# Optimization experiments

Measured on AMD Instinct MI355X. Metric: run time of the kernel, lower is better.

Reference implementation:

```python
import jax, jax.numpy as jnp
import numpy as np

B, S, D, H, L, TPB = 4, 1020, 1024, 16, 4, 17
VOBS, VACT = 4096, 16
DH = D // H
EPS = 1e-3  # keras LayerNormalization default epsilon


def _ln(x, g, b):
    m = jnp.mean(x, axis=-1, keepdims=True)
    v = jnp.mean((x - m) ** 2, axis=-1, keepdims=True)
    return (x - m) * jax.lax.rsqrt(v + EPS) * g + b


def setup_inputs() -> dict:
    key = jax.random.key(0)
    ks = iter(jax.random.split(key, 64))
    def p(shape, s=0.02):
        return jax.random.normal(next(ks), shape, jnp.float32) * s
    pos = np.arange(S)
    is_obs = jnp.asarray((pos % TPB) < (TPB - 1))
    tok = jax.random.randint(next(ks), (B, S), 0, VOBS)
    tok = jnp.where(is_obs[None, :], tok, tok % VACT).astype(jnp.int32)
    d = dict(
        tokens=tok,
        pos_emb=p((S, D)), emb_obs=p((VOBS, D)), emb_act=p((VACT, D)),
        ln1_g=jnp.ones((L, D)), ln1_b=jnp.zeros((L, D)),
        wq=p((L, D, D)), bq=jnp.zeros((L, D)),
        wk=p((L, D, D)), bk=jnp.zeros((L, D)),
        wv=p((L, D, D)), bv=jnp.zeros((L, D)),
        wo=p((L, D, D)), bo=jnp.zeros((L, D)),
        ln2_g=jnp.ones((L, D)), ln2_b=jnp.zeros((L, D)),
        w1=p((L, D, 4 * D)), b1=jnp.zeros((L, 4 * D)),
        w2=p((L, 4 * D, D)), b2=jnp.zeros((L, D)),
        lnf_g=jnp.ones((D,)), lnf_b=jnp.zeros((D,)),
        ho1=p((D, D)), bo1=jnp.zeros((D,)),
        ho2=p((D, VOBS)), bo2=jnp.zeros((VOBS,)),
        he1=p((D, D)), be1=jnp.zeros((D,)),
        he2=p((D, 2)), be2=jnp.zeros((2,)),
    )
    return d


def reference(tokens, pos_emb, emb_obs, emb_act, ln1_g, ln1_b, wq, bq, wk, bk,
              wv, bv, wo, bo, ln2_g, ln2_b, w1, b1, w2, b2, lnf_g, lnf_b,
              ho1, bo1, ho2, bo2, he1, be1, he2, be2):
    pos = jnp.arange(S)
    is_obs = (pos % TPB) < (TPB - 1)  # obs positions within each block
    # token embedding: obs table on obs positions, act table on act positions
    x = jnp.where(is_obs[None, :, None],
                  emb_obs[jnp.minimum(tokens, VOBS - 1)],
                  emb_act[jnp.minimum(tokens, VACT - 1)])
    x = x + pos_emb[None]
    neg_mask = (1.0 - jnp.tril(jnp.ones((S, S), jnp.float32))) * -1e9
    inv_sqrt_dk = 1.0 / np.sqrt(DH).astype(np.float32)
    for i in range(L):
        h = _ln(x, ln1_g[i], ln1_b[i])
        q = (h @ wq[i] + bq[i]).reshape(B, S, H, DH).transpose(0, 2, 1, 3)
        k = (h @ wk[i] + bk[i]).reshape(B, S, H, DH).transpose(0, 2, 1, 3)
        v = (h @ wv[i] + bv[i]).reshape(B, S, H, DH).transpose(0, 2, 1, 3)
        scores = jnp.einsum('bhqd,bhkd->bhqk', q, k) * inv_sqrt_dk + neg_mask
        w = jax.nn.softmax(scores, axis=-1)
        o = jnp.einsum('bhqk,bhkd->bhqd', w, v).transpose(0, 2, 1, 3).reshape(B, S, D)
        x = x + (o @ wo[i] + bo[i])
        h = _ln(x, ln2_g[i], ln2_b[i])
        h = jax.nn.gelu(h @ w1[i] + b1[i], approximate=False) @ w2[i] + b2[i]
        x = x + h
    x = _ln(x, lnf_g, lnf_b)
    # head slices (static)
    p_np = np.arange(S)
    head_obs_idx = jnp.asarray(np.nonzero(((p_np + 1) % TPB) != (TPB - 1))[0])  # 960
    act_idx = jnp.asarray(np.nonzero((p_np % TPB) == (TPB - 1))[0])            # 60
    xo = x[:, head_obs_idx]
    logits_obs = jax.nn.relu(xo @ ho1 + bo1) @ ho2 + bo2   # [B, 960, VOBS]
    xe = x[:, act_idx]
    logits_ends = jax.nn.relu(xe @ he1 + be1) @ he2 + be2  # [B, 60, 2]
    return (logits_obs, logits_ends)
```

## Files before the change

kernel.cpp:

```cpp
#include <hip/hip_runtime.h>
#include <hip/hip_bf16.h>
#include <math.h>

namespace {

constexpr int kS = 1020, kD = 1024, kTPB = 17, kDH = 64;
constexpr int kVOBS = 4096, kVACT = 16;
constexpr int kBS = 4080;
constexpr float kEPS = 1e-3f;

typedef float f32x4 __attribute__((ext_vector_type(4)));
typedef __bf16 bfx8 __attribute__((ext_vector_type(8)));
typedef unsigned short u16;
typedef u16 us8 __attribute__((ext_vector_type(8)));
typedef u16 us4 __attribute__((ext_vector_type(4)));

__device__ __forceinline__ float bf2f(u16 u) {
  union { unsigned int i; float f; } v; v.i = (unsigned int)u << 16; return v.f;
}
__device__ __forceinline__ u16 f2bf(float f) {
  union { float f; unsigned int i; } v; v.f = f;
  unsigned int r = v.i + 0x7FFFu + ((v.i >> 16) & 1u);
  return (u16)(r >> 16);
}

__global__ void k_embed(const int* __restrict__ tokens, const float* __restrict__ pos_emb,
                        const float* __restrict__ emb_obs, const float* __restrict__ emb_act,
                        float* __restrict__ x) {
  int bs = blockIdx.x;
  int s = bs % kS;
  int tk = tokens[bs];
  bool obs = (s % kTPB) < (kTPB - 1);
  const float* e;
  if (obs) { int t2 = tk < kVOBS - 1 ? tk : kVOBS - 1; e = emb_obs + (size_t)t2 * kD; }
  else     { int t2 = tk < kVACT - 1 ? tk : kVACT - 1; e = emb_act + (size_t)t2 * kD; }
  int c = threadIdx.x * 4;
  float4 ev = *(const float4*)(e + c);
  float4 pv = *(const float4*)(pos_emb + (size_t)s * kD + c);
  float4 o; o.x = ev.x + pv.x; o.y = ev.y + pv.y; o.z = ev.z + pv.z; o.w = ev.w + pv.w;
  *(float4*)(x + (size_t)bs * kD + c) = o;
}

__global__ void k_pack_bias(const float* __restrict__ bq, const float* __restrict__ bk,
                            const float* __restrict__ bv, float* __restrict__ bqkv) {
  int idx = blockIdx.x * 256 + threadIdx.x;
  int l = idx / 3072, rem = idx % 3072;
  int sel = rem >> 10, cc = rem & 1023;
  const float* src = sel == 0 ? bq : (sel == 1 ? bk : bv);
  bqkv[idx] = src[l * kD + cc];
}

__global__ void k_ln(const float* __restrict__ x, const float* __restrict__ g,
                     const float* __restrict__ b, u16* __restrict__ out) {
  int row = blockIdx.x;
  int t = threadIdx.x;
  const float* xr = x + (size_t)row * kD;
  float4 v = *(const float4*)(xr + t * 4);
  float s1 = v.x + v.y + v.z + v.w;
  float s2 = v.x * v.x + v.y * v.y + v.z * v.z + v.w * v.w;
  #pragma unroll
  for (int m = 32; m; m >>= 1) { s1 += __shfl_xor(s1, m); s2 += __shfl_xor(s2, m); }
  __shared__ float ls1[4], ls2[4];
  int w = t >> 6;
  if ((t & 63) == 0) { ls1[w] = s1; ls2[w] = s2; }
  __syncthreads();
  float S1 = ls1[0] + ls1[1] + ls1[2] + ls1[3];
  float S2 = ls2[0] + ls2[1] + ls2[2] + ls2[3];
  float mean = S1 * (1.0f / kD);
  float var = S2 * (1.0f / kD) - mean * mean;
  float rs = rsqrtf(var + kEPS);
  int c = t * 4;
  float4 gv = *(const float4*)(g + c);
  float4 bv = *(const float4*)(b + c);
  us4 o;
  o[0] = f2bf((v.x - mean) * rs * gv.x + bv.x);
  o[1] = f2bf((v.y - mean) * rs * gv.y + bv.y);
  o[2] = f2bf((v.z - mean) * rs * gv.z + bv.z);
  o[3] = f2bf((v.w - mean) * rs * gv.w + bv.w);
  *(us4*)(out + (size_t)row * kD + c) = o;
}

__global__ void k_transpose(const float* __restrict__ in, u16* __restrict__ out,
                            int R, int C, int ld) {
  __shared__ float tile[32][33];
  int tx = threadIdx.x, ty = threadIdx.y;
  int c0 = blockIdx.x * 32, r0 = blockIdx.y * 32;
  #pragma unroll
  for (int i = 0; i < 4; ++i)
    tile[ty + i * 8][tx] = in[(size_t)(r0 + ty + i * 8) * ld + c0 + tx];
  __syncthreads();
  #pragma unroll
  for (int i = 0; i < 4; ++i)
    out[(size_t)(c0 + ty + i * 8) * R + r0 + tx] = f2bf(tile[tx][ty + i * 8]);
}

template <int EPI, int BM>
__global__ void __launch_bounds__(256)
k_gemm(const u16* __restrict__ A, const u16* __restrict__ Bt, const float* __restrict__ bias,
       const float* __restrict__ resid, void* __restrict__ out, int M, int N, int K, int ldo) {
  constexpr int MFRAG = BM / 32;
  __shared__ alignas(16) u16 As[BM * 32];
  __shared__ alignas(16) u16 Bs[128 * 32];
  int tid = threadIdx.x;
  int nwg = gridDim.x * gridDim.y;
  int lin = blockIdx.y * gridDim.x + blockIdx.x;
  int swzid = (lin & 7) * (nwg >> 3) + (lin >> 3);
  int m0 = (swzid % gridDim.x) * BM;
  int n0 = (swzid / gridDim.x) * 128;
  int lane = tid & 63, wv = tid >> 6;
  int wm = wv >> 1, wn = wv & 1;
  f32x4 acc[MFRAG][4] = {};

  for (int k0 = 0; k0 < K; k0 += 32) {
    #pragma unroll
    for (int n = 0; n < BM / 64; ++n) {
      int u = n * 256 + wv * 64 + lane;
      int r = u >> 2, ch = u & 3;
      int gr = m0 + r; if (gr >= M) gr = M - 1;
      int cg = ch ^ ((r >> 1) & 3);
      const u16* src = A + (size_t)gr * K + k0 + cg * 8;
      __builtin_amdgcn_global_load_lds(
          (const __attribute__((address_space(1))) unsigned int*)src,
          (__attribute__((address_space(3))) unsigned int*)&As[(size_t)(n * 256 + wv * 64) * 8],
          16, 0, 0);
    }
    #pragma unroll
    for (int n = 0; n < 2; ++n) {
      int u = n * 256 + wv * 64 + lane;
      int r = u >> 2, ch = u & 3;
      int cg = ch ^ ((r >> 1) & 3);
      const u16* src = Bt + (size_t)(n0 + r) * K + k0 + cg * 8;
      __builtin_amdgcn_global_load_lds(
          (const __attribute__((address_space(1))) unsigned int*)src,
          (__attribute__((address_space(3))) unsigned int*)&Bs[(size_t)(n * 256 + wv * 64) * 8],
          16, 0, 0);
    }
    __syncthreads();

    bfx8 af[MFRAG], bfr[4];
    int ch = lane >> 4;
    #pragma unroll
    for (int mf = 0; mf < MFRAG; ++mf) {
      int row = wm * (BM / 2) + mf * 16 + (lane & 15);
      af[mf] = *(const bfx8*)(&As[row * 32 + ((ch ^ ((row >> 1) & 3)) << 3)]);
    }
    #pragma unroll
    for (int nf = 0; nf < 4; ++nf) {
      int row = wn * 64 + nf * 16 + (lane & 15);
      bfr[nf] = *(const bfx8*)(&Bs[row * 32 + ((ch ^ ((row >> 1) & 3)) << 3)]);
    }
    #pragma unroll
    for (int mf = 0; mf < MFRAG; ++mf)
      #pragma unroll
      for (int nf = 0; nf < 4; ++nf)
        acc[mf][nf] = __builtin_amdgcn_mfma_f32_16x16x32_bf16(af[mf], bfr[nf], acc[mf][nf], 0, 0, 0);
    __syncthreads();
  }

  #pragma unroll
  for (int mf = 0; mf < MFRAG; ++mf) {
    #pragma unroll
    for (int nf = 0; nf < 4; ++nf) {
      int gcol = n0 + wn * 64 + nf * 16 + (lane & 15);
      float bv = bias ? bias[gcol] : 0.0f;
      #pragma unroll
      for (int r = 0; r < 4; ++r) {
        int grow = m0 + wm * (BM / 2) + mf * 16 + (lane >> 4) * 4 + r;
        if (grow >= M) continue;
        float val = acc[mf][nf][r] + bv;
        size_t off2 = (size_t)grow * ldo + gcol;
        if (EPI == 0) {
          ((u16*)out)[off2] = f2bf(val);
        } else if (EPI == 1) {
          ((u16*)out)[off2] = f2bf(val > 0.f ? val : 0.f);
        } else if (EPI == 2) {
          ((u16*)out)[off2] = f2bf(0.5f * val * (1.f + erff(val * 0.70710678118654752440f)));
        } else if (EPI == 3) {
          ((float*)out)[off2] = resid[off2] + val;
        } else {
          ((float*)out)[off2] = val;
        }
      }
    }
  }
}

__device__ __forceinline__ int swz(int row, int colu16) {
  return (row * 64 + colu16) ^ ((row & 7) << 3) ^ ((row & 24) << 1);
}

__global__ void __launch_bounds__(256)
k_attn(const u16* __restrict__ q, const u16* __restrict__ k, const u16* __restrict__ v,
       u16* __restrict__ o, int ldin) {
  __shared__ u16 Kl[64 * 64];
  __shared__ u16 Vt[64 * 64];
  const int qb = blockIdx.x * 64;
  const int bh = blockIdx.y;
  const int b = bh >> 4, hh = bh & 15;
  const int tid = threadIdx.x;
  const int lane = tid & 63, w = tid >> 6;
  const int g = lane >> 4, c = lane & 15;
  const int q0 = qb + w * 16;
  const size_t base = (size_t)(b * kS) * ldin + hh * kDH;

  bfx8 qf0, qf1;
  {
    int qr = q0 + c; if (qr >= kS) qr = kS - 1;
    const u16* qp = q + base + (size_t)qr * ldin + g * 8;
    qf0 = *(const bfx8*)(qp);
    qf1 = *(const bfx8*)(qp + 32);
  }

  float mst = -1e30f, lsum = 0.f;
  f32x4 ot[4] = {};

  const int ntiles = blockIdx.x + 1;
  for (int t = 0; t < ntiles; ++t) {
    const int kt = t * 64;
    {
      int kr = tid >> 2, ds2 = (tid & 3) * 16;
      int kg = kt + kr; if (kg >= kS) kg = kS - 1;
      const u16* kp = k + base + (size_t)kg * ldin + ds2;
      us8 a0 = *(const us8*)(kp);
      us8 a1 = *(const us8*)(kp + 8);
      *(us8*)(&Kl[swz(kr, ds2)]) = a0;
      *(us8*)(&Kl[swz(kr, ds2 + 8)]) = a1;
      const u16* vp = v + base + (size_t)kg * ldin + ds2;
      us8 b0 = *(const us8*)(vp);
      us8 b1 = *(const us8*)(vp + 8);
      #pragma unroll
      for (int i2 = 0; i2 < 8; ++i2) Vt[swz(ds2 + i2, kr)] = b0[i2];
      #pragma unroll
      for (int i2 = 0; i2 < 8; ++i2) Vt[swz(ds2 + 8 + i2, kr)] = b1[i2];
    }
    __syncthreads();

    f32x4 s[4];
    #pragma unroll
    for (int kb = 0; kb < 4; ++kb) {
      bfx8 kf0 = *(const bfx8*)(&Kl[swz(kb * 16 + c, g * 8)]);
      bfx8 kf1 = *(const bfx8*)(&Kl[swz(kb * 16 + c, g * 8 + 32)]);
      f32x4 acc = {};
      acc = __builtin_amdgcn_mfma_f32_16x16x32_bf16(kf0, qf0, acc, 0, 0, 0);
      acc = __builtin_amdgcn_mfma_f32_16x16x32_bf16(kf1, qf1, acc, 0, 0, 0);
      s[kb] = acc;
    }

    const int qg = q0 + c;
    const bool diag = (kt + 63 > q0);
    float p[4][4];
    float tmax = -1e30f;
    #pragma unroll
    for (int kb = 0; kb < 4; ++kb)
      #pragma unroll
      for (int r = 0; r < 4; ++r) {
        float val = s[kb][r] * 0.125f;
        if (diag && (kt + kb * 16 + g * 4 + r > qg)) val = -1e30f;
        p[kb][r] = val;
        tmax = fmaxf(tmax, val);
      }
    tmax = fmaxf(tmax, __shfl_xor(tmax, 16));
    tmax = fmaxf(tmax, __shfl_xor(tmax, 32));
    float mnew = fmaxf(mst, tmax);
    float alpha = __expf(mst - mnew);
    float psum = 0.f;
    #pragma unroll
    for (int kb = 0; kb < 4; ++kb)
      #pragma unroll
      for (int r = 0; r < 4; ++r) {
        float e = __expf(p[kb][r] - mnew);
        p[kb][r] = e;
        psum += e;
      }
    psum += __shfl_xor(psum, 16);
    psum += __shfl_xor(psum, 32);
    lsum = lsum * alpha + psum;
    mst = mnew;
    #pragma unroll
    for (int db = 0; db < 4; ++db) {
      ot[db][0] *= alpha; ot[db][1] *= alpha;
      ot[db][2] *= alpha; ot[db][3] *= alpha;
    }

    #pragma unroll
    for (int h = 0; h < 2; ++h) {
      bfx8 pf;
      #pragma unroll
      for (int j = 0; j < 8; ++j)
        pf[j] = (__bf16)p[2 * h + (j >> 2)][j & 3];
      #pragma unroll
      for (int db = 0; db < 4; ++db) {
        us4 lo = *(const us4*)(&Vt[swz(16 * db + c, 32 * h + 4 * g)]);
        us4 hi = *(const us4*)(&Vt[swz(16 * db + c, 32 * h + 16 + 4 * g)]);
        union { us8 u; bfx8 bf; } cv;
        cv.u[0] = lo[0]; cv.u[1] = lo[1]; cv.u[2] = lo[2]; cv.u[3] = lo[3];
        cv.u[4] = hi[0]; cv.u[5] = hi[1]; cv.u[6] = hi[2]; cv.u[7] = hi[3];
        ot[db] = __builtin_amdgcn_mfma_f32_16x16x32_bf16(cv.bf, pf, ot[db], 0, 0, 0);
      }
    }
    __syncthreads();
  }

  if (q0 + c < kS) {
    float inv = 1.0f / lsum;
    u16* op = o + (size_t)(b * kS) * kD + hh * kDH + (size_t)(q0 + c) * kD;
    #pragma unroll
    for (int db = 0; db < 4; ++db)
      #pragma unroll
      for (int r = 0; r < 4; ++r)
        op[16 * db + 4 * g + r] = f2bf(ot[db][r] * inv);
  }
}

__global__ void k_gather_obs(const u16* __restrict__ xf, u16* __restrict__ xo) {
  int r = blockIdx.x;
  int b = r / 960, rr = r % 960;
  int j = rr & 15, blk = rr >> 4;
  int s = blk * kTPB + j + (j == 15 ? 1 : 0);
  const unsigned int* src = (const unsigned int*)(xf + ((size_t)(b * kS + s)) * kD);
  unsigned int* dst = (unsigned int*)(xo + (size_t)r * kD);
  dst[threadIdx.x] = src[threadIdx.x];
  dst[threadIdx.x + 256] = src[threadIdx.x + 256];
}
__global__ void k_gather_act(const u16* __restrict__ xf, u16* __restrict__ xe) {
  int r = blockIdx.x;
  int b = r / 60, rr = r % 60;
  int s = rr * kTPB + (kTPB - 1);
  const unsigned int* src = (const unsigned int*)(xf + ((size_t)(b * kS + s)) * kD);
  unsigned int* dst = (unsigned int*)(xe + (size_t)r * kD);
  dst[threadIdx.x] = src[threadIdx.x];
  dst[threadIdx.x + 256] = src[threadIdx.x + 256];
}

__global__ void k_ends(const u16* __restrict__ t2, const float* __restrict__ he2,
                       const float* __restrict__ be2, float* __restrict__ out) {
  int r = blockIdx.x;
  int t = threadIdx.x;
  float p0 = 0.f, p1 = 0.f;
  for (int j = t; j < kD; j += 256) {
    float xv = bf2f(t2[(size_t)r * kD + j]);
    p0 += xv * he2[j * 2];
    p1 += xv * he2[j * 2 + 1];
  }
  #pragma unroll
  for (int msk = 32; msk; msk >>= 1) { p0 += __shfl_xor(p0, msk); p1 += __shfl_xor(p1, msk); }
  __shared__ float l0[4], l1[4];
  int w = t >> 6;
  if ((t & 63) == 0) { l0[w] = p0; l1[w] = p1; }
  __syncthreads();
  if (t == 0) {
    out[r * 2 + 0] = l0[0] + l0[1] + l0[2] + l0[3] + be2[0];
    out[r * 2 + 1] = l1[0] + l1[1] + l1[2] + l1[3] + be2[1];
  }
}

}

extern "C" void kernel_launch(void* const* d_in, const int* in_sizes, int n_in,
                              void* d_out, int out_size, void* d_ws, size_t ws_size,
                              hipStream_t stream) {
  const int*   tokens  = (const int*)  d_in[0];
  const float* pos_emb = (const float*)d_in[1];
  const float* emb_obs = (const float*)d_in[2];
  const float* emb_act = (const float*)d_in[3];
  const float* ln1_g = (const float*)d_in[4];
  const float* ln1_b = (const float*)d_in[5];
  const float* wq = (const float*)d_in[6];
  const float* bq = (const float*)d_in[7];
  const float* wk = (const float*)d_in[8];
  const float* bk = (const float*)d_in[9];
  const float* wv = (const float*)d_in[10];
  const float* bv = (const float*)d_in[11];
  const float* wo = (const float*)d_in[12];
  const float* bo = (const float*)d_in[13];
  const float* ln2_g = (const float*)d_in[14];
  const float* ln2_b = (const float*)d_in[15];
  const float* w1 = (const float*)d_in[16];
  const float* b1 = (const float*)d_in[17];
  const float* w2 = (const float*)d_in[18];
  const float* b2 = (const float*)d_in[19];
  const float* lnf_g = (const float*)d_in[20];
  const float* lnf_b = (const float*)d_in[21];
  const float* ho1 = (const float*)d_in[22];
  const float* bo1 = (const float*)d_in[23];
  const float* ho2 = (const float*)d_in[24];
  const float* bo2 = (const float*)d_in[25];
  const float* he1 = (const float*)d_in[26];
  const float* be1 = (const float*)d_in[27];
  const float* he2 = (const float*)d_in[28];
  const float* be2 = (const float*)d_in[29];
  (void)in_sizes; (void)n_in; (void)out_size; (void)ws_size;

  char* ws = (char*)d_ws;
  size_t off = 0;
  auto alloc = [&](size_t bytes) -> char* {
    char* p = ws + off; off += (bytes + 255) & ~(size_t)255; return p;
  };
  u16*   wTbig = (u16*)alloc((size_t)4096 * 1024 * 2);
  float* x  = (float*)alloc((size_t)kBS * kD * 4);
  u16*   h  = (u16*)alloc((size_t)kBS * kD * 2);
  char*  scr = alloc((size_t)kBS * 4096 * 2);
  float* bqkv = (float*)alloc((size_t)4 * 3072 * 4);
  const size_t slotB = (size_t)kBS * kD * 2;
  u16* qkv = (u16*)scr;
  u16* ob  = (u16*)(scr + (size_t)kBS * 3072 * 2);
  u16* mid = (u16*)scr;
  u16* xf = (u16*)scr;
  u16* xo = (u16*)(scr + slotB);
  u16* t1 = (u16*)(scr + 2 * slotB);
  u16* xe = (u16*)(scr + 3 * slotB);
  u16* t2 = (u16*)(scr + 3 * slotB + (size_t)240 * kD * 2 + 256);

  dim3 tb(32, 8);
  dim3 tg(32, 32);
  k_embed<<<kBS, 256, 0, stream>>>(tokens, pos_emb, emb_obs, emb_act, x);
  k_pack_bias<<<48, 256, 0, stream>>>(bq, bk, bv, bqkv);

  for (int i = 0; i < 4; ++i) {
    const size_t wOff = (size_t)i * kD * kD;
    k_ln<<<kBS, 256, 0, stream>>>(x, ln1_g + i * kD, ln1_b + i * kD, h);

    k_transpose<<<tg, tb, 0, stream>>>(wq + wOff, wTbig, 1024, 1024, 1024);
    k_transpose<<<tg, tb, 0, stream>>>(wk + wOff, wTbig + (size_t)1024 * 1024, 1024, 1024, 1024);
    k_transpose<<<tg, tb, 0, stream>>>(wv + wOff, wTbig + (size_t)2048 * 1024, 1024, 1024, 1024);
    k_gemm<0, 128><<<dim3(32, 24), 256, 0, stream>>>(h, wTbig, bqkv + i * 3072, nullptr, qkv,
                                                     kBS, 3072, 1024, 3072);

    k_attn<<<dim3(16, 64), 256, 0, stream>>>(qkv, qkv + 1024, qkv + 2048, ob, 3072);

    k_transpose<<<tg, tb, 0, stream>>>(wo + wOff, wTbig, 1024, 1024, 1024);
    k_gemm<3, 64><<<dim3(64, 8), 256, 0, stream>>>(ob, wTbig, bo + i * kD, x, x,
                                                   kBS, 1024, 1024, 1024);

    k_ln<<<kBS, 256, 0, stream>>>(x, ln2_g + i * kD, ln2_b + i * kD, h);

    for (int c = 0; c < 4; ++c)
      k_transpose<<<tg, tb, 0, stream>>>(w1 + (size_t)i * kD * 4096 + c * 1024,
                                         wTbig + (size_t)c * 1024 * 1024, 1024, 1024, 4096);
    k_gemm<2, 128><<<dim3(32, 32), 256, 0, stream>>>(h, wTbig, b1 + (size_t)i * 4096, nullptr,
                                                     mid, kBS, 4096, 1024, 4096);
    k_transpose<<<dim3(32, 128), tb, 0, stream>>>(w2 + (size_t)i * 4096 * kD, wTbig,
                                                  4096, 1024, 1024);
    k_gemm<3, 64><<<dim3(64, 8), 256, 0, stream>>>(mid, wTbig, b2 + i * kD, x, x,
                                                   kBS, 1024, 4096, 1024);
  }

  k_ln<<<kBS, 256, 0, stream>>>(x, lnf_g, lnf_b, xf);
  k_gather_obs<<<3840, 256, 0, stream>>>(xf, xo);
  k_gather_act<<<240, 256, 0, stream>>>(xf, xe);

  k_transpose<<<tg, tb, 0, stream>>>(ho1, wTbig, 1024, 1024, 1024);
  k_gemm<1, 64><<<dim3(60, 8), 256, 0, stream>>>(xo, wTbig, bo1, nullptr, t1,
                                                 3840, 1024, 1024, 1024);
  for (int c = 0; c < 4; ++c)
    k_transpose<<<tg, tb, 0, stream>>>(ho2 + c * 1024, wTbig + (size_t)c * 1024 * 1024,
                                       1024, 1024, 4096);
  k_gemm<4, 128><<<dim3(30, 32), 256, 0, stream>>>(t1, wTbig, bo2, nullptr,
                                                   (float*)d_out, 3840, 4096, 1024, 4096);
  k_transpose<<<tg, tb, 0, stream>>>(he1, wTbig, 1024, 1024, 1024);
  k_gemm<1, 64><<<dim3(4, 8), 256, 0, stream>>>(xe, wTbig, be1, nullptr, t2,
                                                240, 1024, 1024, 1024);
  k_ends<<<240, 256, 0, stream>>>(t2, he2, be2, (float*)d_out + (size_t)3840 * 4096);
}
```

Before: 1.458 ms.

## Double-buffer GEMM LDS tiles and drop workgroup swizzle

The GEMM kernel now keeps two LDS buffers for the A and B tiles. It issues global-to-LDS loads for the next K step before running the MFMAs on the current one, so memory latency can overlap with compute. It also removes the grouped workgroup-ID swizzle in favour of a plain blockIdx mapping, which may change L2 reuse across workgroups. Doubling LDS per block can lower occupancy. Whether the loop-end sync still orders the async LDS writes correctly depends on code not shown.

Result: faster. 1.377 ms (-5.6%).

```diff
diff --git a/kernel.cpp b/kernel.cpp
--- a/kernel.cpp
+++ b/kernel.cpp
@@ -99,55 +99,58 @@
 k_gemm(const u16* __restrict__ A, const u16* __restrict__ Bt, const float* __restrict__ bias,
        const float* __restrict__ resid, void* __restrict__ out, int M, int N, int K, int ldo) {
   constexpr int MFRAG = BM / 32;
-  __shared__ alignas(16) u16 As[BM * 32];
-  __shared__ alignas(16) u16 Bs[128 * 32];
+  __shared__ alignas(16) u16 As[2][BM * 32];
+  __shared__ alignas(16) u16 Bs[2][128 * 32];
   int tid = threadIdx.x;
-  int nwg = gridDim.x * gridDim.y;
-  int lin = blockIdx.y * gridDim.x + blockIdx.x;
-  int swzid = (lin & 7) * (nwg >> 3) + (lin >> 3);
-  int m0 = (swzid % gridDim.x) * BM;
-  int n0 = (swzid / gridDim.x) * 128;
+  int m0 = blockIdx.x * BM, n0 = blockIdx.y * 128;
   int lane = tid & 63, wv = tid >> 6;
   int wm = wv >> 1, wn = wv & 1;
   f32x4 acc[MFRAG][4] = {};
 
-  for (int k0 = 0; k0 < K; k0 += 32) {
+  auto stage = [&](int buf, int k0) {
     #pragma unroll
     for (int n = 0; n < BM / 64; ++n) {
-      int u = n * 256 + wv * 64 + lane;
+      int u = n * 256 + tid;
       int r = u >> 2, ch = u & 3;
       int gr = m0 + r; if (gr >= M) gr = M - 1;
       int cg = ch ^ ((r >> 1) & 3);
       const u16* src = A + (size_t)gr * K + k0 + cg * 8;
       __builtin_amdgcn_global_load_lds(
           (const __attribute__((address_space(1))) unsigned int*)src,
-          (__attribute__((address_space(3))) unsigned int*)&As[(size_t)(n * 256 + wv * 64) * 8],
+          (__attribute__((address_space(3))) unsigned int*)&As[buf][(n * 256 + wv * 64) * 8],
           16, 0, 0);
     }
     #pragma unroll
     for (int n = 0; n < 2; ++n) {
-      int u = n * 256 + wv * 64 + lane;
+      int u = n * 256 + tid;
       int r = u >> 2, ch = u & 3;
       int cg = ch ^ ((r >> 1) & 3);
       const u16* src = Bt + (size_t)(n0 + r) * K + k0 + cg * 8;
       __builtin_amdgcn_global_load_lds(
           (const __attribute__((address_space(1))) unsigned int*)src,
-          (__attribute__((address_space(3))) unsigned int*)&Bs[(size_t)(n * 256 + wv * 64) * 8],
+          (__attribute__((address_space(3))) unsigned int*)&Bs[buf][(n * 256 + wv * 64) * 8],
           16, 0, 0);
     }
-    __syncthreads();
+  };
+
+  stage(0, 0);
+  __syncthreads();
+  const int nk = K >> 5;
+  for (int t = 0; t < nk; ++t) {
+    int cur = t & 1;
+    if (t + 1 < nk) stage(cur ^ 1, (t + 1) << 5);
 
     bfx8 af[MFRAG], bfr[4];
     int ch = lane >> 4;
     #pragma unroll
     for (int mf = 0; mf < MFRAG; ++mf) {
       int row = wm * (BM / 2) + mf * 16 + (lane & 15);
-      af[mf] = *(const bfx8*)(&As[row * 32 + ((ch ^ ((row >> 1) & 3)) << 3)]);
+      af[mf] = *(const bfx8*)(&As[cur][row * 32 + ((ch ^ ((row >> 1) & 3)) << 3)]);
     }
     #pragma unroll
     for (int nf = 0; nf < 4; ++nf) {
       int row = wn * 64 + nf * 16 + (lane & 15);
-      bfr[nf] = *(const bfx8*)(&Bs[row * 32 + ((ch ^ ((row >> 1) & 3)) << 3)]);
+      bfr[nf] = *(const bfx8*)(&Bs[cur][row * 32 + ((ch ^ ((row >> 1) & 3)) << 3)]);
     }
     #pragma unroll
     for (int mf = 0; mf < MFRAG; ++mf)
```
